# Performance work log

Hardware: AMD Instinct MI355X
Metric: run time of the kernel (lower is better)

## Reference

```python
import jax, jax.numpy as jnp
import numpy as np

B, T, D, H, L, F = 32, 512, 1024, 1024, 2, 256  # batch, time, input dim, units, layers, feature_size


def setup_inputs() -> dict:
    key = jax.random.key(0)
    ks = jax.random.split(key, 9)
    s_in = 1.0 / np.sqrt(D)
    s_h = 1.0 / np.sqrt(H)
    x = jax.random.normal(ks[0], (B, T, D), dtype=jnp.float32)
    # Stacked LSTM params: gate order [i, f, g, o] concatenated along last axis.
    Wx = jax.random.normal(ks[1], (L, D, 4 * H), dtype=jnp.float32) * s_in
    Wh = jax.random.normal(ks[2], (L, H, 4 * H), dtype=jnp.float32) * s_h
    b = jnp.zeros((L, 4 * H), dtype=jnp.float32)
    # Output heads.
    Wmu = jax.random.normal(ks[3], (H, F), dtype=jnp.float32) * s_h
    bmu = jnp.zeros((F,), dtype=jnp.float32)
    Wls = jax.random.normal(ks[4], (H, F), dtype=jnp.float32) * s_h
    bls = jnp.zeros((F,), dtype=jnp.float32)
    y_min = jnp.zeros((F,), dtype=jnp.float32)  # y_min init arg (0.0 broadcast)
    return {"x": x, "Wx": Wx, "Wh": Wh, "b": b, "Wmu": Wmu, "bmu": bmu,
            "Wls": Wls, "bls": bls, "y_min": y_min}


def _lstm_layer(x, Wx, Wh, b):
    # x: [B, T, Din]; Wx: [Din, 4H]; Wh: [H, 4H]; b: [4H]
    Bn = x.shape[0]
    Hn = Wh.shape[0]
    # Precompute input projections for all timesteps (one big GEMM).
    x_proj = jnp.einsum('btd,dg->btg', x, Wx) + b  # [B, T, 4H]

    def step(carry, xp):
        h, c = carry
        g = xp + h @ Wh  # [B, 4H]
        i, f, gg, o = jnp.split(g, 4, axis=-1)
        c = jax.nn.sigmoid(f) * c + jax.nn.sigmoid(i) * jnp.tanh(gg)
        h = jax.nn.sigmoid(o) * jnp.tanh(c)
        return (h, c), h

    h0 = jnp.zeros((Bn, Hn), dtype=x.dtype)
    c0 = jnp.zeros((Bn, Hn), dtype=x.dtype)
    _, hs = jax.lax.scan(step, (h0, c0), jnp.swapaxes(x_proj, 0, 1))  # hs: [T, B, H]
    return jnp.swapaxes(hs, 0, 1)  # [B, T, H]


def reference(x, Wx, Wh, b, Wmu, bmu, Wls, bls, y_min):
    for l in range(Wx.shape[0]):  # small fixed n_layers loop
        x = _lstm_layer(x, Wx[l], Wh[l], b[l])
    mu = jax.nn.softplus(x @ Wmu + bmu) + y_min  # [B, T, F]
    log_sigma = x @ Wls + bls                    # [B, T, F]
    return (mu, log_sigma)
```

## Files before the change

### kernel.cpp

```cpp
#include <hip/hip_runtime.h>

typedef unsigned short u16;
typedef unsigned int   u32;
typedef unsigned long long u64;
typedef short s16x4 __attribute__((ext_vector_type(4)));
typedef short s16x8 __attribute__((ext_vector_type(8)));
typedef float f32x4 __attribute__((ext_vector_type(4)));
typedef u32   u32x4 __attribute__((ext_vector_type(4)));

#define GK 1024

__device__ inline u16 f2bf(float f) {
    u32 u = __builtin_bit_cast(u32, f);
    u += 0x7FFFu + ((u >> 16) & 1u);
    return (u16)(u >> 16);
}
__device__ inline u16 f2h(float f) {
    _Float16 h = (_Float16)f;
    return __builtin_bit_cast(u16, h);
}
__device__ inline float h2f(u16 u) {
    return (float)__builtin_bit_cast(_Float16, u);
}
__device__ inline float fast_sigmoid(float x) {
    return __builtin_amdgcn_rcpf(1.f + __expf(-x));
}
__device__ inline float fast_tanh(float x) {
    return 1.f - 2.f * __builtin_amdgcn_rcpf(1.f + __expf(2.f * x));
}
__device__ inline f32x4 mfma16(s16x8 a, s16x8 b, f32x4 c) {
    return __builtin_amdgcn_mfma_f32_16x16x32_bf16(a, b, c, 0, 0, 0);
}
__device__ inline s16x8 mk8(s16x4 lo, s16x4 hi) {
    return __builtin_shufflevector(lo, hi, 0, 1, 2, 3, 4, 5, 6, 7);
}
__device__ inline u64 ald(const u16* p) {
    return __hip_atomic_load((const u64*)p, __ATOMIC_RELAXED, __HIP_MEMORY_SCOPE_AGENT);
}

__global__ void k_f2bf(const float* __restrict__ in, u16* __restrict__ out, int n) {
    int i = (blockIdx.x * 256 + threadIdx.x) * 4;
    if (i < n) {
        float4 v = *(const float4*)(in + i);
        ushort4 o;
        o.x = f2bf(v.x); o.y = f2bf(v.y); o.z = f2bf(v.z); o.w = f2bf(v.w);
        *(ushort4*)(out + i) = o;
    }
}

__global__ void k_transpose_bf(const float* __restrict__ in, u16* __restrict__ out,
                               int R, int C) {
    __shared__ float tile[32][33];
    int tid = threadIdx.x;
    int xs = (tid & 7) * 4;
    int y  = tid >> 3;
    int r0 = blockIdx.y * 32, c0 = blockIdx.x * 32;
    float4 v = *(const float4*)(in + (size_t)(r0 + y) * C + c0 + xs);
    tile[y][xs + 0] = v.x; tile[y][xs + 1] = v.y;
    tile[y][xs + 2] = v.z; tile[y][xs + 3] = v.w;
    __syncthreads();
    ushort4 o;
    o.x = f2bf(tile[xs + 0][y]); o.y = f2bf(tile[xs + 1][y]);
    o.z = f2bf(tile[xs + 2][y]); o.w = f2bf(tile[xs + 3][y]);
    *(ushort4*)(out + (size_t)(c0 + y) * R + r0 + xs) = o;
}

__global__ void k_unpack(const u16* __restrict__ in, u16* __restrict__ out) {
    int idx = blockIdx.x * 256 + threadIdx.x;
    int slot = idx >> 12;
    int c = idx & 4095;
    int q = c >> 7, b = (c >> 2) & 31, ri = c & 3;
    const u16* p = in + (size_t)(slot + 1) * 32768 + q * 1024 + b * 32 + ri * 8;
    u64 lo = *(const u64*)p;
    u64 hi = *(const u64*)(p + 4);
    u16* o = out + (size_t)(slot * 32 + b) * 1024 + q * 32 + ri * 4;
    *(u64*)o = lo;
    *(u64*)(o + 16) = hi;
}

template<int MODE>
__launch_bounds__(256, 2)
__global__ void k_gemm(const u16* __restrict__ A, const u16* __restrict__ BT,
                       const float* __restrict__ bias,
                       u16* __restrict__ Cb, float* __restrict__ Cf,
                       const float* __restrict__ b2, const float* __restrict__ ymin,
                       int gridN) {
    int bid = blockIdx.x;
    int m0 = (bid / gridN) * 128, n0 = (bid % gridN) * 128;
    __shared__ u16 As[128 * 40];
    __shared__ u16 Bs[128 * 40];
    int tid = threadIdx.x;
    int lane = tid & 63, w = tid >> 6;
    int wr = w >> 1, wc = w & 1;
    int rr = lane & 15, r16 = lane >> 4;
    f32x4 acc[4][4] = {};
    for (int kt = 0; kt < GK / 32; ++kt) {
        int k0 = kt * 32;
#pragma unroll
        for (int it = 0; it < 2; ++it) {
            int idx = it * 256 + tid;
            int row = idx >> 2, ch = idx & 3;
            *(u32x4*)(&As[row * 40 + ch * 8]) =
                *(const u32x4*)(A + (size_t)(m0 + row) * GK + k0 + ch * 8);
            *(u32x4*)(&Bs[row * 40 + ch * 8]) =
                *(const u32x4*)(BT + (size_t)(n0 + row) * GK + k0 + ch * 8);
        }
        __syncthreads();
        s16x8 af[4], bfr[4];
#pragma unroll
        for (int i = 0; i < 4; ++i) {
            int abase = (wr * 64 + i * 16 + rr) * 40 + r16 * 4;
            af[i] = mk8(*(const s16x4*)(&As[abase]), *(const s16x4*)(&As[abase + 16]));
            int bbase = (wc * 64 + i * 16 + rr) * 40 + r16 * 4;
            bfr[i] = mk8(*(const s16x4*)(&Bs[bbase]), *(const s16x4*)(&Bs[bbase + 16]));
        }
#pragma unroll
        for (int i = 0; i < 4; ++i)
#pragma unroll
            for (int j = 0; j < 4; ++j)
                acc[i][j] = mfma16(af[i], bfr[j], acc[i][j]);
        __syncthreads();
    }
#pragma unroll
    for (int i = 0; i < 4; ++i) {
#pragma unroll
        for (int j = 0; j < 4; ++j) {
#pragma unroll
            for (int r = 0; r < 4; ++r) {
                int m = m0 + wr * 64 + i * 16 + r16 * 4 + r;
                int n = n0 + wc * 64 + j * 16 + rr;
                float v = acc[i][j][r];
                if (MODE == 0) {
                    v += bias[n];
                    int orow = (m & 511) * 32 + (m >> 9);
                    int colx = ((n & 1023) << 2) | (n >> 10);
                    Cb[(size_t)orow * 4096 + colx] = f2h(v);
                } else {
                    int orow = (m & 31) * 512 + (m >> 5);
                    if (n < 256) {
                        v += bias[n];
                        float sp = fmaxf(v, 0.f) + log1pf(expf(-fabsf(v)));
                        Cf[(size_t)orow * 256 + n] = sp + ymin[n];
                    } else {
                        v += b2[n - 256];
                        Cf[4194304 + (size_t)orow * 256 + (n - 256)] = v;
                    }
                }
            }
        }
    }
}

__launch_bounds__(512, 1)
__global__ void k_fused(const u16* __restrict__ Wh0T, const u16* __restrict__ Wx1T,
                        const u16* __restrict__ Wh1T, const u16* __restrict__ xproj,
                        const float* __restrict__ b1,
                        u16* __restrict__ hseq0, u16* __restrict__ hseq1,
                        u32* __restrict__ flags) {
    __shared__ u16 wlds[2][32][2][64][8];
    __shared__ f32x4 part[2][2][4][64];
    int tid = threadIdx.x, blk = blockIdx.x;
    int lane = tid & 63, w = tid >> 6;
    int grp = w >> 2, wl = w & 3;
    int mt = wl >> 1, qh = wl & 1;
    int u0 = blk * 8;
    int rr = lane & 15, r16 = lane >> 4;

    if (wl < 2) {
        int ntp = wl;
        int cg = (rr & 3) * 1024 + u0 + ntp * 4 + (rr >> 2);
        const u16* wsrc = (grp == 0 ? Wh0T : Wh1T) + (size_t)cg * GK + r16 * 4;
#pragma unroll
        for (int q = 0; q < 32; ++q) {
            *(s16x8*)(&wlds[grp][q][ntp][lane][0]) =
                mk8(*(const s16x4*)(wsrc + q * 32), *(const s16x4*)(wsrc + q * 32 + 16));
        }
    }
    u64 wpx_u = (u64)(uintptr_t)(Wx1T +
        (size_t)((rr & 3) * 1024 + u0 + (rr >> 2)) * GK + r16 * 4);

    int b_ = mt * 16 + (lane >> 4) * 4 + (lane & 3);
    int uu = (lane >> 2) & 3;
    int unit = u0 + qh * 4 + uu;
    float c0 = 0.f, c1 = 0.f;
    float b1r[4];
#pragma unroll
    for (int g = 0; g < 4; ++g) b1r[g] = b1[g * 1024 + unit];
    const u16* xp = xproj + (size_t)b_ * 4096 + (size_t)unit * 4;

    int sblk = blk & 3;
    const int soff = (blk >> 2) * 1024 + b_ * 32 + (((sblk & 1) * 2 + qh) * 8 + (sblk >> 1) * 4);
    const int cbase = qh * 16384 + mt * 512 + rr * 32 + r16 * 8;

    __syncthreads();

    for (int r = 0; r <= 512; ++r) {
        if (w == 0) {
            u32 tgt = (u32)r;
            while (true) {
                u32 v0 = __hip_atomic_load(&flags[lane], __ATOMIC_RELAXED,
                                           __HIP_MEMORY_SCOPE_AGENT);
                u32 v1 = __hip_atomic_load(&flags[64 + lane], __ATOMIC_RELAXED,
                                           __HIP_MEMORY_SCOPE_AGENT);
                if (__all((v0 >= tgt) & (v1 >= tgt))) break;
                __builtin_amdgcn_s_sleep(1);
            }
        }
        __syncthreads();
        __builtin_amdgcn_sched_barrier(0);

        f32x4 a0[2] = {}, a1[2] = {};
        u64 xv = 0;
        if (grp == 0) {
            if (r < 512) xv = *(const u64*)(xp + (size_t)r * 131072);
            asm volatile("" : "+v"(wpx_u));
            const u16* wpx = (const u16*)(uintptr_t)wpx_u;
            const u16* hp = hseq0 + (size_t)r * 32768 + cbase;
#pragma unroll
            for (int c = 0; c < 4; ++c) {
                u64 lo4[4], hi4[4];
                s16x8 bx0[4], bx1[4];
#pragma unroll
                for (int j = 0; j < 4; ++j) {
                    int jj = c * 4 + j;
                    int q = qh * 16 + jj;
                    lo4[j] = ald(hp + jj * 1024);
                    hi4[j] = ald(hp + jj * 1024 + 4);
                    const u16* bp = wpx + q * 32;
                    bx0[j] = mk8(*(const s16x4*)bp, *(const s16x4*)(bp + 16));
                    bx1[j] = mk8(*(const s16x4*)(bp + 4096),
                                 *(const s16x4*)(bp + 4096 + 16));
                }
#pragma unroll
                for (int j = 0; j < 4; ++j) {
                    int q = qh * 16 + c * 4 + j;
                    s16x8 a = mk8(__builtin_bit_cast(s16x4, lo4[j]),
                                  __builtin_bit_cast(s16x4, hi4[j]));
                    a0[0] = mfma16(a, *(const s16x8*)(&wlds[0][q][0][lane][0]), a0[0]);
                    a0[1] = mfma16(a, *(const s16x8*)(&wlds[0][q][1][lane][0]), a0[1]);
                    a1[0] = mfma16(a, bx0[j], a1[0]);
                    a1[1] = mfma16(a, bx1[j], a1[1]);
                }
            }
            part[mt][1 - qh][0][lane] = a0[1 - qh];
            part[mt][1 - qh][1][lane] = a1[1 - qh];
        } else {
            if (r > 0) {
                const u16* hp = hseq1 + (size_t)(r - 1) * 32768 + cbase;
#pragma unroll
                for (int c = 0; c < 4; ++c) {
                    u64 lo4[4], hi4[4];
#pragma unroll
                    for (int j = 0; j < 4; ++j) {
                        int jj = c * 4 + j;
                        lo4[j] = ald(hp + jj * 1024);
                        hi4[j] = ald(hp + jj * 1024 + 4);
                    }
#pragma unroll
                    for (int j = 0; j < 4; ++j) {
                        int q = qh * 16 + c * 4 + j;
                        s16x8 a = mk8(__builtin_bit_cast(s16x4, lo4[j]),
                                      __builtin_bit_cast(s16x4, hi4[j]));
                        a0[0] = mfma16(a, *(const s16x8*)(&wlds[1][q][0][lane][0]), a0[0]);
                        a0[1] = mfma16(a, *(const s16x8*)(&wlds[1][q][1][lane][0]), a0[1]);
                    }
                }
            }
            part[mt][0][2 + qh][lane] = a0[0];
            part[mt][1][2 + qh][lane] = a0[1];
        }
        __syncthreads();

        if (grp == 0) {
            if (r < 512) {
                f32x4 acc = a0[qh] + part[mt][qh][0][lane];
                float r0 = acc[0], r1 = acc[1], r2 = acc[2], r3 = acc[3];
                float x0 = __shfl_xor(r0, 1), x1 = __shfl_xor(r1, 1);
                float x2 = __shfl_xor(r2, 1), x3 = __shfl_xor(r3, 1);
                bool o1 = lane & 1;
                float s0 = o1 ? x1 : r0, s1 = o1 ? r1 : x0;
                float s2 = o1 ? x3 : r2, s3 = o1 ? r3 : x2;
                float y0 = __shfl_xor(s0, 2), y1 = __shfl_xor(s1, 2);
                float y2 = __shfl_xor(s2, 2), y3 = __shfl_xor(s3, 2);
                bool o2 = lane & 2;
                float gi = (o2 ? y2 : s0) + h2f((u16)(xv));
                float gf = (o2 ? y3 : s1) + h2f((u16)(xv >> 16));
                float gg = (o2 ? s2 : y0) + h2f((u16)(xv >> 32));
                float go = (o2 ? s3 : y1) + h2f((u16)(xv >> 48));
                float I  = fast_sigmoid(gi);
                float Fg = fast_sigmoid(gf);
                float G  = fast_tanh(gg);
                float O  = fast_sigmoid(go);
                c0 = Fg * c0 + I * G;
                u32 hq = (u32)f2bf(O * fast_tanh(c0));
                u32 o4 = (u32)__shfl_xor((int)hq, 4);
                u32 m32 = (lane & 4) ? ((o4 & 0xffffu) | (hq << 16))
                                     : ((hq & 0xffffu) | (o4 << 16));
                u32 o8 = (u32)__shfl_xor((int)m32, 8);
                u64 m64 = (lane & 8) ? (((u64)o8) | ((u64)m32 << 32))
                                     : (((u64)m32) | ((u64)o8 << 32));
                if ((lane & 12) == 0)
                    __hip_atomic_store((u64*)(hseq0 + (size_t)(r + 1) * 32768 + soff),
                                       m64, __ATOMIC_RELAXED, __HIP_MEMORY_SCOPE_AGENT);
            }
            if (r > 0) {
                f32x4 acc = a1[qh] + part[mt][qh][1][lane]
                          + part[mt][qh][2][lane] + part[mt][qh][3][lane];
                float r0 = acc[0], r1 = acc[1], r2 = acc[2], r3 = acc[3];
                float x0 = __shfl_xor(r0, 1), x1 = __shfl_xor(r1, 1);
                float x2 = __shfl_xor(r2, 1), x3 = __shfl_xor(r3, 1);
                bool o1 = lane & 1;
                float s0 = o1 ? x1 : r0, s1 = o1 ? r1 : x0;
                float s2 = o1 ? x3 : r2, s3 = o1 ? r3 : x2;
                float y0 = __shfl_xor(s0, 2), y1 = __shfl_xor(s1, 2);
                float y2 = __shfl_xor(s2, 2), y3 = __shfl_xor(s3, 2);
                bool o2 = lane & 2;
                float gi = (o2 ? y2 : s0) + b1r[0];
                float gf = (o2 ? y3 : s1) + b1r[1];
                float gg = (o2 ? s2 : y0) + b1r[2];
                float go = (o2 ? s3 : y1) + b1r[3];
                float I  = fast_sigmoid(gi);
                float Fg = fast_sigmoid(gf);
                float G  = fast_tanh(gg);
                float O  = fast_sigmoid(go);
                c1 = Fg * c1 + I * G;
                u32 hq = (u32)f2bf(O * fast_tanh(c1));
                u32 o4 = (u32)__shfl_xor((int)hq, 4);
                u32 m32 = (lane & 4) ? ((o4 & 0xffffu) | (hq << 16))
                                     : ((hq & 0xffffu) | (o4 << 16));
                u32 o8 = (u32)__shfl_xor((int)m32, 8);
                u64 m64 = (lane & 8) ? (((u64)o8) | ((u64)m32 << 32))
                                     : (((u64)m32) | ((u64)o8 << 32));
                if ((lane & 12) == 0)
                    __hip_atomic_store((u64*)(hseq1 + (size_t)r * 32768 + soff),
                                       m64, __ATOMIC_RELAXED, __HIP_MEMORY_SCOPE_AGENT);
            }
        }
        __syncthreads();
        if (tid == 0)
            __hip_atomic_store(&flags[blk], (u32)(r + 1), __ATOMIC_RELAXED,
                               __HIP_MEMORY_SCOPE_AGENT);
    }
}

extern "C" void kernel_launch(void* const* d_in, const int* in_sizes, int n_in,
                              void* d_out, int out_size, void* d_ws, size_t ws_size,
                              hipStream_t stream) {
    const float* x   = (const float*)d_in[0];
    const float* Wx  = (const float*)d_in[1];
    const float* Wh  = (const float*)d_in[2];
    const float* b   = (const float*)d_in[3];
    const float* Wmu = (const float*)d_in[4];
    const float* bmu = (const float*)d_in[5];
    const float* Wls = (const float*)d_in[6];
    const float* bls = (const float*)d_in[7];
    const float* ym  = (const float*)d_in[8];
    float* out = (float*)d_out;

    char* ws = (char*)d_ws;
    u16* hseq0 = (u16*)(ws);
    u16* xbf   = (u16*)(ws);
    u16* hseq1 = (u16*)(ws + 33619968);
    u16* wxT   = (u16*)(ws + 67239936);
    u16* whT   = (u16*)(ws + 84017152);
    u16* whdT  = (u16*)(ws + 100794368);
    u16* xproj = (u16*)(ws + 101842944);
    u16* h1lin = xproj;
    u32* flags = (u32*)(ws + 236060672);

    k_f2bf<<<16384, 256, 0, stream>>>(x, xbf, 16777216);
    dim3 tg(128, 32);
    k_transpose_bf<<<tg, 256, 0, stream>>>(Wx,           wxT,           1024, 4096);
    k_transpose_bf<<<tg, 256, 0, stream>>>(Wx + 4194304, wxT + 4194304, 1024, 4096);
    k_transpose_bf<<<tg, 256, 0, stream>>>(Wh,           whT,           1024, 4096);
    k_transpose_bf<<<tg, 256, 0, stream>>>(Wh + 4194304, whT + 4194304, 1024, 4096);
    dim3 hg(8, 32);
    k_transpose_bf<<<hg, 256, 0, stream>>>(Wmu, whdT,          1024, 256);
    k_transpose_bf<<<hg, 256, 0, stream>>>(Wls, whdT + 262144, 1024, 256);

    k_gemm<0><<<4096, 256, 0, stream>>>(xbf, wxT, b, xproj, nullptr, nullptr, nullptr, 32);

    hipMemsetAsync(hseq0, 0, 65536, stream);
    hipMemsetAsync(hseq1, 0, 65536, stream);
    hipMemsetAsync(flags, 0, 512, stream);

    k_fused<<<128, 512, 0, stream>>>(whT, wxT + 4194304, whT + 4194304, xproj,
                                     b + 4096, hseq0, hseq1, flags);

    k_unpack<<<8192, 256, 0, stream>>>(hseq1, h1lin);
    k_gemm<1><<<512, 256, 0, stream>>>(h1lin, whdT, bmu, nullptr, out, bls, ym, 4);
}
```

Measured before the change: 8.216 ms.

## Halve persistent LSTM grid, stream repacked weights from global with 16-byte h loads

The persistent fused two-layer LSTM kernel now runs on 64 blocks with 16 hidden units each instead of 128 blocks with 8. Recurrent weights are no longer staged in LDS; they are repacked in place by a new pre-pass kernel so each lane reads contiguous 16-byte fragments straight from global memory and cache. Hidden-state loads become single dwordx4 loads with sc1, and the flag poll covers only 64 entries. Fewer blocks means cheaper cross-block synchronisation each step, at the cost of twice the MFMA work per block and weight reads that now depend on cache hits instead of LDS.

```diff
diff --git a/kernel.cpp b/kernel.cpp
--- a/kernel.cpp
+++ b/kernel.cpp
@@ -34,9 +34,13 @@
 __device__ inline s16x8 mk8(s16x4 lo, s16x4 hi) {
     return __builtin_shufflevector(lo, hi, 0, 1, 2, 3, 4, 5, 6, 7);
 }
-__device__ inline u64 ald(const u16* p) {
-    return __hip_atomic_load((const u64*)p, __ATOMIC_RELAXED, __HIP_MEMORY_SCOPE_AGENT);
-}
+__device__ inline u32x4 ald16(const u16* p) {
+    u32x4 v;
+    asm volatile("global_load_dwordx4 %0, %1, off sc1" : "=v"(v) : "v"(p));
+    return v;
+}
+#define HWAIT() do { asm volatile("s_waitcnt vmcnt(0)" ::: "memory"); \
+                     __builtin_amdgcn_sched_barrier(0); } while (0)
 
 __global__ void k_f2bf(const float* __restrict__ in, u16* __restrict__ out, int n) {
     int i = (blockIdx.x * 256 + threadIdx.x) * 4;
@@ -63,6 +67,15 @@
     o.x = f2bf(tile[xs + 0][y]); o.y = f2bf(tile[xs + 1][y]);
     o.z = f2bf(tile[xs + 2][y]); o.w = f2bf(tile[xs + 3][y]);
     *(ushort4*)(out + (size_t)(c0 + y) * R + r0 + xs) = o;
+}
+
+__global__ void k_wpackip(u16* __restrict__ wm) {
+    int idx = blockIdx.x * 256 + threadIdx.x;
+    u64* p = (u64*)(wm + (size_t)idx * 32);
+    u64 w0 = p[0], w1 = p[1], w2 = p[2], w3 = p[3];
+    u64 w4 = p[4], w5 = p[5], w6 = p[6], w7 = p[7];
+    p[0] = w0; p[1] = w4; p[2] = w1; p[3] = w5;
+    p[4] = w2; p[5] = w6; p[6] = w3; p[7] = w7;
 }
 
 __global__ void k_unpack(const u16* __restrict__ in, u16* __restrict__ out) {
@@ -151,189 +164,162 @@
     }
 }
 
+__device__ inline float lstm_core(f32x4 acc, float ai, float af, float ag, float ao,
+                                  float& c, int lane) {
+    float r0 = acc[0], r1 = acc[1], r2 = acc[2], r3 = acc[3];
+    float x0 = __shfl_xor(r0, 1), x1 = __shfl_xor(r1, 1);
+    float x2 = __shfl_xor(r2, 1), x3 = __shfl_xor(r3, 1);
+    bool o1 = lane & 1;
+    float s0 = o1 ? x1 : r0, s1 = o1 ? r1 : x0;
+    float s2 = o1 ? x3 : r2, s3 = o1 ? r3 : x2;
+    float y0 = __shfl_xor(s0, 2), y1 = __shfl_xor(s1, 2);
+    float y2 = __shfl_xor(s2, 2), y3 = __shfl_xor(s3, 2);
+    bool o2 = lane & 2;
+    float gi = (o2 ? y2 : s0) + ai;
+    float gf = (o2 ? y3 : s1) + af;
+    float gg = (o2 ? s2 : y0) + ag;
+    float go = (o2 ? s3 : y1) + ao;
+    float I  = fast_sigmoid(gi);
+    float Fg = fast_sigmoid(gf);
+    float G  = fast_tanh(gg);
+    float O  = fast_sigmoid(go);
+    c = Fg * c + I * G;
+    return O * fast_tanh(c);
+}
+__device__ inline void pack_store(float h, int lane, u16* dst) {
+    u32 hq = (u32)f2bf(h);
+    u32 o4 = (u32)__shfl_xor((int)hq, 4);
+    u32 m32 = (lane & 4) ? ((o4 & 0xffffu) | (hq << 16))
+                         : ((hq & 0xffffu) | (o4 << 16));
+    u32 o8 = (u32)__shfl_xor((int)m32, 8);
+    u64 m64 = (lane & 8) ? (((u64)o8) | ((u64)m32 << 32))
+                         : (((u64)m32) | ((u64)o8 << 32));
+    if ((lane & 12) == 0)
+        __hip_atomic_store((u64*)dst, m64, __ATOMIC_RELAXED, __HIP_MEMORY_SCOPE_AGENT);
+}
+
 __launch_bounds__(512, 1)
-__global__ void k_fused(const u16* __restrict__ Wh0T, const u16* __restrict__ Wx1T,
-                        const u16* __restrict__ Wh1T, const u16* __restrict__ xproj,
+__global__ void k_fused(const u16* __restrict__ Wp0, const u16* __restrict__ Wpx,
+                        const u16* __restrict__ Wp1, const u16* __restrict__ xproj,
                         const float* __restrict__ b1,
                         u16* __restrict__ hseq0, u16* __restrict__ hseq1,
                         u32* __restrict__ flags) {
-    __shared__ u16 wlds[2][32][2][64][8];
-    __shared__ f32x4 part[2][2][4][64];
+    __shared__ f32x4 part[2][4][4][64];
     int tid = threadIdx.x, blk = blockIdx.x;
     int lane = tid & 63, w = tid >> 6;
     int grp = w >> 2, wl = w & 3;
     int mt = wl >> 1, qh = wl & 1;
-    int u0 = blk * 8;
     int rr = lane & 15, r16 = lane >> 4;
 
-    if (wl < 2) {
-        int ntp = wl;
-        int cg = (rr & 3) * 1024 + u0 + ntp * 4 + (rr >> 2);
-        const u16* wsrc = (grp == 0 ? Wh0T : Wh1T) + (size_t)cg * GK + r16 * 4;
-#pragma unroll
-        for (int q = 0; q < 32; ++q) {
-            *(s16x8*)(&wlds[grp][q][ntp][lane][0]) =
-                mk8(*(const s16x4*)(wsrc + q * 32), *(const s16x4*)(wsrc + q * 32 + 16));
-        }
-    }
-    u64 wpx_u = (u64)(uintptr_t)(Wx1T +
-        (size_t)((rr & 3) * 1024 + u0 + (rr >> 2)) * GK + r16 * 4);
+    const u16* wsB[4];
+    const u16* wsX[4];
+#pragma unroll
+    for (int ct = 0; ct < 4; ++ct) {
+        size_t cg = (size_t)((rr & 3) * 1024 + blk * 16 + ct * 4 + (rr >> 2));
+        size_t off = cg * GK + qh * 512 + r16 * 8;
+        wsB[ct] = (grp ? Wp1 : Wp0) + off;
+        wsX[ct] = Wpx + off;
+    }
 
     int b_ = mt * 16 + (lane >> 4) * 4 + (lane & 3);
     int uu = (lane >> 2) & 3;
-    int unit = u0 + qh * 4 + uu;
-    float c0 = 0.f, c1 = 0.f;
-    float b1r[4];
-#pragma unroll
-    for (int g = 0; g < 4; ++g) b1r[g] = b1[g * 1024 + unit];
-    const u16* xp = xproj + (size_t)b_ * 4096 + (size_t)unit * 4;
-
-    int sblk = blk & 3;
-    const int soff = (blk >> 2) * 1024 + b_ * 32 + (((sblk & 1) * 2 + qh) * 8 + (sblk >> 1) * 4);
+    int ue[2];
+    ue[0] = blk * 16 + (qh * 2) * 4 + uu;
+    ue[1] = ue[0] + 4;
+    float b1r[2][4];
+#pragma unroll
+    for (int e = 0; e < 2; ++e)
+#pragma unroll
+        for (int g = 0; g < 4; ++g) b1r[e][g] = b1[g * 1024 + ue[e]];
+    const u16* xpe0 = xproj + (size_t)b_ * 4096 + (size_t)ue[0] * 4;
+    const u16* xpe1 = xproj + (size_t)b_ * 4096 + (size_t)ue[1] * 4;
+    float c0[2] = {0.f, 0.f}, c1[2] = {0.f, 0.f};
+
+    int qs = blk >> 1, ps = blk & 1;
     const int cbase = qh * 16384 + mt * 512 + rr * 32 + r16 * 8;
-
-    __syncthreads();
 
     for (int r = 0; r <= 512; ++r) {
         if (w == 0) {
-            u32 tgt = (u32)r;
+            const u32* fp = flags + lane;
             while (true) {
-                u32 v0 = __hip_atomic_load(&flags[lane], __ATOMIC_RELAXED,
-                                           __HIP_MEMORY_SCOPE_AGENT);
-                u32 v1 = __hip_atomic_load(&flags[64 + lane], __ATOMIC_RELAXED,
-                                           __HIP_MEMORY_SCOPE_AGENT);
-                if (__all((v0 >= tgt) & (v1 >= tgt))) break;
+                u32 v;
+                asm volatile("global_load_dword %0, %1, off sc1\n\ts_waitcnt vmcnt(0)"
+                             : "=v"(v) : "v"(fp) : "memory");
+                if (__all((int)(v >= (u32)r))) break;
                 __builtin_amdgcn_s_sleep(1);
             }
         }
         __syncthreads();
         __builtin_amdgcn_sched_barrier(0);
 
-        f32x4 a0[2] = {}, a1[2] = {};
-        u64 xv = 0;
+        f32x4 acc0[4] = {}, acc1[4] = {};
+        u64 xv0 = 0, xv1 = 0;
         if (grp == 0) {
-            if (r < 512) xv = *(const u64*)(xp + (size_t)r * 131072);
-            asm volatile("" : "+v"(wpx_u));
-            const u16* wpx = (const u16*)(uintptr_t)wpx_u;
+            if (r < 512) {
+                xv0 = *(const u64*)(xpe0 + (size_t)r * 131072);
+                xv1 = *(const u64*)(xpe1 + (size_t)r * 131072);
+            }
             const u16* hp = hseq0 + (size_t)r * 32768 + cbase;
-#pragma unroll
-            for (int c = 0; c < 4; ++c) {
-                u64 lo4[4], hi4[4];
-                s16x8 bx0[4], bx1[4];
-#pragma unroll
-                for (int j = 0; j < 4; ++j) {
-                    int jj = c * 4 + j;
-                    int q = qh * 16 + jj;
-                    lo4[j] = ald(hp + jj * 1024);
-                    hi4[j] = ald(hp + jj * 1024 + 4);
-                    const u16* bp = wpx + q * 32;
-                    bx0[j] = mk8(*(const s16x4*)bp, *(const s16x4*)(bp + 16));
-                    bx1[j] = mk8(*(const s16x4*)(bp + 4096),
-                                 *(const s16x4*)(bp + 4096 + 16));
-                }
-#pragma unroll
-                for (int j = 0; j < 4; ++j) {
-                    int q = qh * 16 + c * 4 + j;
-                    s16x8 a = mk8(__builtin_bit_cast(s16x4, lo4[j]),
-                                  __builtin_bit_cast(s16x4, hi4[j]));
-                    a0[0] = mfma16(a, *(const s16x8*)(&wlds[0][q][0][lane][0]), a0[0]);
-                    a0[1] = mfma16(a, *(const s16x8*)(&wlds[0][q][1][lane][0]), a0[1]);
-                    a1[0] = mfma16(a, bx0[j], a1[0]);
-                    a1[1] = mfma16(a, bx1[j], a1[1]);
-                }
-            }
-            part[mt][1 - qh][0][lane] = a0[1 - qh];
-            part[mt][1 - qh][1][lane] = a1[1 - qh];
+            u32x4 hf[16];
+#pragma unroll
+            for (int jj = 0; jj < 16; ++jj) hf[jj] = ald16(hp + jj * 1024);
+            HWAIT();
+#pragma unroll
+            for (int jj = 0; jj < 16; ++jj) {
+                s16x8 a = __builtin_bit_cast(s16x8, hf[jj]);
+#pragma unroll
+                for (int ct = 0; ct < 4; ++ct) {
+                    acc0[ct] = mfma16(a, *(const s16x8*)(wsB[ct] + jj * 32), acc0[ct]);
+                    acc1[ct] = mfma16(a, *(const s16x8*)(wsX[ct] + jj * 32), acc1[ct]);
+                }
+            }
+            int o0 = (1 - qh) * 2;
+            part[mt][o0][0][lane]     = acc0[o0];
+            part[mt][o0 + 1][0][lane] = acc0[o0 + 1];
+            part[mt][o0][1][lane]     = acc1[o0];
+            part[mt][o0 + 1][1][lane] = acc1[o0 + 1];
         } else {
             if (r > 0) {
                 const u16* hp = hseq1 + (size_t)(r - 1) * 32768 + cbase;
-#pragma unroll
-                for (int c = 0; c < 4; ++c) {
-                    u64 lo4[4], hi4[4];
-#pragma unroll
-                    for (int j = 0; j < 4; ++j) {
-                        int jj = c * 4 + j;
-                        lo4[j] = ald(hp + jj * 1024);
-                        hi4[j] = ald(hp + jj * 1024 + 4);
-                    }
-#pragma unroll
-                    for (int j = 0; j < 4; ++j) {
-                        int q = qh * 16 + c * 4 + j;
-                        s16x8 a = mk8(__builtin_bit_cast(s16x4, lo4[j]),
-                                      __builtin_bit_cast(s16x4, hi4[j]));
-                        a0[0] = mfma16(a, *(const s16x8*)(&wlds[1][q][0][lane][0]), a0[0]);
-                        a0[1] = mfma16(a, *(const s16x8*)(&wlds[1][q][1][lane][0]), a0[1]);
-                    }
-                }
-            }
-            part[mt][0][2 + qh][lane] = a0[0];
-            part[mt][1][2 + qh][lane] = a0[1];
+                u32x4 hf[16];
+#pragma unroll
+                for (int jj = 0; jj < 16; ++jj) hf[jj] = ald16(hp + jj * 1024);
+                HWAIT();
+#pragma unroll
+                for (int jj = 0; jj < 16; ++jj) {
+                    s16x8 a = __builtin_bit_cast(s16x8, hf[jj]);
+#pragma unroll
+                    for (int ct = 0; ct < 4; ++ct)
+                        acc0[ct] = mfma16(a, *(const s16x8*)(wsB[ct] + jj * 32), acc0[ct]);
+                }
+            }
+#pragma unroll
+            for (int ct = 0; ct < 4; ++ct)
+                part[mt][ct][2 + qh][lane] = acc0[ct];
         }
         __syncthreads();
 
         if (grp == 0) {
-            if (r < 512) {
-                f32x4 acc = a0[qh] + part[mt][qh][0][lane];
-                float r0 = acc[0], r1 = acc[1], r2 = acc[2], r3 = acc[3];
-                float x0 = __shfl_xor(r0, 1), x1 = __shfl_xor(r1, 1);
-                float x2 = __shfl_xor(r2, 1), x3 = __shfl_xor(r3, 1);
-                bool o1 = lane & 1;
-                float s0 = o1 ? x1 : r0, s1 = o1 ? r1 : x0;
-                float s2 = o1 ? x3 : r2, s3 = o1 ? r3 : x2;
-                float y0 = __shfl_xor(s0, 2), y1 = __shfl_xor(s1, 2);
-                float y2 = __shfl_xor(s2, 2), y3 = __shfl_xor(s3, 2);
-                bool o2 = lane & 2;
-                float gi = (o2 ? y2 : s0) + h2f((u16)(xv));
-                float gf = (o2 ? y3 : s1) + h2f((u16)(xv >> 16));
-                float gg = (o2 ? s2 : y0) + h2f((u16)(xv >> 32));
-                float go = (o2 ? s3 : y1) + h2f((u16)(xv >> 48));
-                float I  = fast_sigmoid(gi);
-                float Fg = fast_sigmoid(gf);
-                float G  = fast_tanh(gg);
-                float O  = fast_sigmoid(go);
-                c0 = Fg * c0 + I * G;
-                u32 hq = (u32)f2bf(O * fast_tanh(c0));
-                u32 o4 = (u32)__shfl_xor((int)hq, 4);
-                u32 m32 = (lane & 4) ? ((o4 & 0xffffu) | (hq << 16))
-                                     : ((hq & 0xffffu) | (o4 << 16));
-                u32 o8 = (u32)__shfl_xor((int)m32, 8);
-                u64 m64 = (lane & 8) ? (((u64)o8) | ((u64)m32 << 32))
-                                     : (((u64)m32) | ((u64)o8 << 32));
-                if ((lane & 12) == 0)
-                    __hip_atomic_store((u64*)(hseq0 + (size_t)(r + 1) * 32768 + soff),
-                                       m64, __ATOMIC_RELAXED, __HIP_MEMORY_SCOPE_AGENT);
-            }
-            if (r > 0) {
-                f32x4 acc = a1[qh] + part[mt][qh][1][lane]
-                          + part[mt][qh][2][lane] + part[mt][qh][3][lane];
-                float r0 = acc[0], r1 = acc[1], r2 = acc[2], r3 = acc[3];
-                float x0 = __shfl_xor(r0, 1), x1 = __shfl_xor(r1, 1);
-                float x2 = __shfl_xor(r2, 1), x3 = __shfl_xor(r3, 1);
-                bool o1 = lane & 1;
-                float s0 = o1 ? x1 : r0, s1 = o1 ? r1 : x0;
-                float s2 = o1 ? x3 : r2, s3 = o1 ? r3 : x2;
-                float y0 = __shfl_xor(s0, 2), y1 = __shfl_xor(s1, 2);
-                float y2 = __shfl_xor(s2, 2), y3 = __shfl_xor(s3, 2);
-                bool o2 = lane & 2;
-                float gi = (o2 ? y2 : s0) + b1r[0];
-                float gf = (o2 ? y3 : s1) + b1r[1];
-                float gg = (o2 ? s2 : y0) + b1r[2];
-                float go = (o2 ? s3 : y1) + b1r[3];
-                float I  = fast_sigmoid(gi);
-                float Fg = fast_sigmoid(gf);
-                float G  = fast_tanh(gg);
-                float O  = fast_sigmoid(go);
-                c1 = Fg * c1 + I * G;
-                u32 hq = (u32)f2bf(O * fast_tanh(c1));
-                u32 o4 = (u32)__shfl_xor((int)hq, 4);
-                u32 m32 = (lane & 4) ? ((o4 & 0xffffu) | (hq << 16))
-                                     : ((hq & 0xffffu) | (o4 << 16));
-                u32 o8 = (u32)__shfl_xor((int)m32, 8);
-                u64 m64 = (lane & 8) ? (((u64)o8) | ((u64)m32 << 32))
-                                     : (((u64)m32) | ((u64)o8 << 32));
-                if ((lane & 12) == 0)
-                    __hip_atomic_store((u64*)(hseq1 + (size_t)r * 32768 + soff),
-                                       m64, __ATOMIC_RELAXED, __HIP_MEMORY_SCOPE_AGENT);
+#pragma unroll
+            for (int e = 0; e < 2; ++e) {
+                int ct = qh * 2 + e;
+                u64 xv = e ? xv1 : xv0;
+                if (r < 512) {
+                    f32x4 acc = acc0[ct] + part[mt][ct][0][lane];
+                    float h = lstm_core(acc, h2f((u16)xv), h2f((u16)(xv >> 16)),
+                                        h2f((u16)(xv >> 32)), h2f((u16)(xv >> 48)),
+                                        c0[e], lane);
+                    pack_store(h, lane, hseq0 + (size_t)(r + 1) * 32768
+                               + qs * 1024 + b_ * 32 + ct * 8 + ps * 4);
+                }
+                if (r > 0) {
+                    f32x4 acc = acc1[ct] + part[mt][ct][1][lane]
+                              + part[mt][ct][2][lane] + part[mt][ct][3][lane];
+                    float h = lstm_core(acc, b1r[e][0], b1r[e][1], b1r[e][2], b1r[e][3],
+                                        c1[e], lane);
+                    pack_store(h, lane, hseq1 + (size_t)r * 32768
+                               + qs * 1024 + b_ * 32 + ct * 8 + ps * 4);
+                }
             }
         }
         __syncthreads();
@@ -380,12 +366,15 @@
 
     k_gemm<0><<<4096, 256, 0, stream>>>(xbf, wxT, b, xproj, nullptr, nullptr, nullptr, 32);
 
+    k_wpackip<<<1024, 256, 0, stream>>>(whT);
+    k_wpackip<<<512, 256, 0, stream>>>(wxT + 4194304);
+
     hipMemsetAsync(hseq0, 0, 65536, stream);
     hipMemsetAsync(hseq1, 0, 65536, stream);
     hipMemsetAsync(flags, 0, 512, stream);
 
-    k_fused<<<128, 512, 0, stream>>>(whT, wxT + 4194304, whT + 4194304, xproj,
-                                     b + 4096, hseq0, hseq1, flags);
+    k_fused<<<64, 512, 0, stream>>>(whT, wxT + 4194304, whT + 4194304, xproj,
+                                    b + 4096, hseq0, hseq1, flags);
 
     k_unpack<<<8192, 256, 0, stream>>>(hseq1, h1lin);
     k_gemm<1><<<512, 256, 0, stream>>>(h1lin, whdT, bmu, nullptr, out, bls, ym, 4);
```

After: 15.27 ms. +85.9%, slower.
